# Kernel tuning notes

Hardware: AMD Instinct MI355X
Metric: run time of the kernel (lower is better)

The kernel has to match this reference:

```python
import jax, jax.numpy as jnp
import numpy as np
from jax import lax

C = 768
CA = C // 4  # adapter_channels = 192
L = 197      # 1 CLS + 14*14 patches
T_FRAMES = 16
B = 16
N = B * T_FRAMES


def quick_gelu(x):
    return x * jax.nn.sigmoid(1.702 * x)


def setup_inputs() -> dict:
    key = jax.random.key(0)
    ks = jax.random.split(key, 16)
    s = 0.02
    return {
        "x": jax.random.normal(ks[0], (L, N, C), dtype=jnp.float32),
        "T": T_FRAMES,
        # main path (fc1 -> depthwise conv1d over T -> fc2)
        "fc1_w": jax.random.normal(ks[1], (C, CA), jnp.float32) * s,
        "fc1_b": jnp.zeros((CA,), jnp.float32),
        "conv_w": jax.random.normal(ks[2], (CA, 1, 3), jnp.float32) * s,  # (O, I/g, K)
        "conv_b": jnp.zeros((CA,), jnp.float32),
        "fc2_w": jax.random.normal(ks[3], (CA, C), jnp.float32) * s,
        "fc2_b": jnp.zeros((C,), jnp.float32),
        # offset adapter (fc1 -> depthwise conv3d (1,3,3) -> fc2)
        "off_fc1_w": jax.random.normal(ks[4], (C, CA), jnp.float32) * s,
        "off_fc1_b": jnp.zeros((CA,), jnp.float32),
        "off_conv_w": jax.random.normal(ks[5], (CA, 1, 1, 3, 3), jnp.float32) * s,  # (O, I/g, D, H, W)
        "off_conv_b": jnp.zeros((CA,), jnp.float32),
        "off_fc2_w": jax.random.normal(ks[6], (CA, C), jnp.float32) * s,
        "off_fc2_b": jnp.zeros((C,), jnp.float32),
        # mlp branch (c_in -> QuickGELU -> c_out)
        "mlp_in_w": jax.random.normal(ks[7], (C, CA), jnp.float32) * s,
        "mlp_in_b": jnp.zeros((CA,), jnp.float32),
        "mlp_out_w": jax.random.normal(ks[8], (CA, C), jnp.float32) * s,
        "mlp_out_b": jnp.zeros((C,), jnp.float32),
    }


def _offset_adapter(x, T, fc1_w, fc1_b, conv_w, conv_b, fc2_w, fc2_b):
    Lx, Nx, Cx = x.shape
    Bx = Nx // T
    HW = Lx - 1
    H = int(round(HW ** 0.5))
    Ca = fc1_w.shape[1]
    xp = jnp.transpose(x, (1, 0, 2))            # (N, L, C)
    xs = xp[:, 1:, :].reshape(Bx, T, HW, Cx)    # (B, T, HW, C)
    # former frame: index [0, 0, 1, ..., T-2]
    x_former = jnp.concatenate([xs[:, :1], xs[:, :-1]], axis=1)
    off = xs - x_former
    off = off @ fc1_w + fc1_b                   # (B, T, HW, Ca)
    off = off.reshape(Bx, T, H, H, Ca).transpose(0, 4, 1, 2, 3)  # (B, Ca, T, H, W)
    off = lax.conv_general_dilated(
        off, conv_w, window_strides=(1, 1, 1),
        padding=[(0, 0), (1, 1), (1, 1)],
        dimension_numbers=("NCDHW", "OIDHW", "NCDHW"),
        feature_group_count=Ca,
    ) + conv_b[None, :, None, None, None]
    off = off.transpose(0, 2, 3, 4, 1).reshape(Nx, HW, Ca)
    off = off @ fc2_w + fc2_b                   # (N, L-1, C)
    return jnp.transpose(off, (1, 0, 2))        # (L-1, N, C)


def reference(x, T, fc1_w, fc1_b, conv_w, conv_b, fc2_w, fc2_b,
              off_fc1_w, off_fc1_b, off_conv_w, off_conv_b, off_fc2_w, off_fc2_b,
              mlp_in_w, mlp_in_b, mlp_out_w, mlp_out_b):
    Lx, Nx, Cx = x.shape
    Bx = Nx // T
    Ca = fc1_w.shape[1]

    offset = _offset_adapter(x, T, off_fc1_w, off_fc1_b, off_conv_w, off_conv_b,
                             off_fc2_w, off_fc2_b)  # (L-1, N, C)

    # mlp identity branch
    x_id = quick_gelu(x @ mlp_in_w + mlp_in_b) @ mlp_out_w + mlp_out_b  # (L, N, C)

    # main branch: fc1 -> depthwise conv1d along T -> fc2
    h = x @ fc1_w + fc1_b                                   # (L, N, Ca)
    h = jnp.transpose(h, (1, 0, 2)).reshape(Bx, T, Lx, Ca)  # (B, T, L, Ca)
    h = h.transpose(0, 2, 3, 1).reshape(Bx * Lx, Ca, T)     # (B*L, Ca, T)
    h = lax.conv_general_dilated(
        h, conv_w, window_strides=(1,), padding=[(1, 1)],
        dimension_numbers=("NCH", "OIH", "NCH"),
        feature_group_count=Ca,
    ) + conv_b[None, :, None]
    h = h.transpose(0, 2, 1).reshape(Bx, Lx, T, Ca)
    h = h.transpose(0, 2, 1, 3).reshape(Nx, Lx, Ca)
    h = jnp.transpose(h, (1, 0, 2))                         # (L, N, Ca)
    h = h @ fc2_w + fc2_b                                   # (L, N, C)

    x_id = x_id.at[1:].add(offset)
    return h + x_id
```

## Files before the change

kernel.cpp:

```cpp
#include <hip/hip_runtime.h>

#define L_DIM 197
#define N_DIM 256
#define C_DIM 768
#define CA_DIM 192
#define M_DIM (L_DIM * N_DIM)

typedef short s16x8 __attribute__((ext_vector_type(8)));
typedef float f32x4 __attribute__((ext_vector_type(4)));

__device__ __forceinline__ unsigned short f2bf(float f) {
  unsigned x = __builtin_bit_cast(unsigned, f);
  x = (x + 0x7fffu + ((x >> 16) & 1u)) >> 16;
  return (unsigned short)x;
}
__device__ __forceinline__ float bflo(unsigned u) { return __builtin_bit_cast(float, u << 16); }
__device__ __forceinline__ float bfhi(unsigned u) { return __builtin_bit_cast(float, u & 0xffff0000u); }

__device__ __forceinline__ void unp8(uint4 v, float* f) {
  f[0] = bflo(v.x); f[1] = bfhi(v.x); f[2] = bflo(v.y); f[3] = bfhi(v.y);
  f[4] = bflo(v.z); f[5] = bfhi(v.z); f[6] = bflo(v.w); f[7] = bfhi(v.w);
}

__device__ __forceinline__ void mfma16(f32x4& acc, s16x8 a, s16x8 b) {
  asm("v_mfma_f32_16x16x32_bf16 %0, %1, %2, %0" : "+v"(acc) : "v"(a), "v"(b));
}

typedef const void __attribute__((address_space(1)))* gp_t;
typedef void __attribute__((address_space(3)))* lp_t;
__device__ __forceinline__ void gl16(const void* g, void* l) {
  __builtin_amdgcn_global_load_lds((gp_t)g, (lp_t)l, 16, 0, 0);
}

#define WAITVM(n) asm volatile("s_waitcnt vmcnt(" #n ")" ::: "memory")

__device__ __forceinline__ int swz(int pid, int nwg) {
  const int q = nwg >> 3, r = nwg & 7, x = pid & 7, s = pid >> 3;
  return (x < r ? x * (q + 1) : r * (q + 1) + (x - r) * q) + s;
}

__global__ __launch_bounds__(256) void prep_k(
    const float* __restrict__ fc1_w, const float* __restrict__ mlp_in_w,
    const float* __restrict__ off_fc1_w, const float* __restrict__ fc2_w,
    const float* __restrict__ mlp_out_w, const float* __restrict__ off_fc2_w,
    unsigned short* __restrict__ wa, unsigned short* __restrict__ wc) {
  __shared__ float t[32][33];
  const int b = blockIdx.x;
  const int job = b / 144, tt = b - job * 144;
  const float* in = job == 0 ? fc1_w : job == 1 ? mlp_in_w : job == 2 ? off_fc1_w
                  : job == 3 ? fc2_w : job == 4 ? mlp_out_w : off_fc2_w;
  const int Cc = job < 3 ? 192 : 768;
  const int tc = Cc >> 5;
  const int tr0 = (tt / tc) << 5, tc0 = (tt - (tt / tc) * tc) << 5;
  const int lr = threadIdx.x >> 5, lc = threadIdx.x & 31;
#pragma unroll
  for (int p = 0; p < 4; p++)
    t[p * 8 + lr][lc] = in[(tr0 + p * 8 + lr) * Cc + tc0 + lc];
  __syncthreads();
#pragma unroll
  for (int p = 0; p < 4; p++) {
    const int orow = tc0 + p * 8 + lr;
    const int ocol = tr0 + lc;
    const unsigned short v = f2bf(t[lc][p * 8 + lr]);
    if (job < 3) wa[(job * 192 + orow) * 768 + ocol] = v;
    else         wc[orow * 576 + (job - 3) * 192 + ocol] = v;
  }
}

__global__ __launch_bounds__(256) void xcvt_k(const float* __restrict__ x,
                                              unsigned short* __restrict__ xb) {
  const int total8 = M_DIM * C_DIM / 8;
  const int step = gridDim.x * 256;
  for (int i = blockIdx.x * 256 + threadIdx.x; i < total8; i += step) {
    const float4 a = *(const float4*)(x + (size_t)i * 8);
    const float4 b = *(const float4*)(x + (size_t)i * 8 + 4);
    s16x8 v;
    v[0] = (short)f2bf(a.x); v[1] = (short)f2bf(a.y);
    v[2] = (short)f2bf(a.z); v[3] = (short)f2bf(a.w);
    v[4] = (short)f2bf(b.x); v[5] = (short)f2bf(b.y);
    v[6] = (short)f2bf(b.z); v[7] = (short)f2bf(b.w);
    *(s16x8*)(xb + (size_t)i * 8) = v;
  }
}

__global__ __launch_bounds__(256, 1) void gemm_a_k(
    const unsigned short* __restrict__ xb, const unsigned short* __restrict__ wa,
    const float* __restrict__ fc1_b, const float* __restrict__ mlp_in_b,
    const float* __restrict__ cw, const float* __restrict__ cb,
    const float* __restrict__ off_b1, unsigned short* __restrict__ hcat) {
  __shared__ unsigned short As[3][128 * 32];
  __shared__ unsigned short Bs[3][192 * 32];
  const int tid = threadIdx.x, lane = tid & 63, w = tid >> 6;
  const int lid = swz(blockIdx.x, 3 * 394);
  const int by = lid / 3, bx = lid - by * 3;
  const int m0 = by * 128, n0 = bx * 192;

  const int sr = tid >> 2, sc = (tid & 3) * 8;
  const unsigned short* gA0 = xb + (size_t)(m0 + sr) * C_DIM + sc;
  const unsigned short* gA1 = xb + (size_t)(m0 + 64 + sr) * C_DIM + sc;
  const unsigned short* gB = wa + (size_t)(n0 + sr) * C_DIM + sc;

  auto stage = [&](int kt, int b) {
    gl16(gA0 + kt * 32, &As[b][sr * 32 + sc]);
    gl16(gA1 + kt * 32, &As[b][(64 + sr) * 32 + sc]);
    const unsigned short* pb = gB + kt * 32;
    gl16(pb,               &Bs[b][sr * 32 + sc]);
    gl16(pb + 64 * C_DIM,  &Bs[b][(64 + sr) * 32 + sc]);
    gl16(pb + 128 * C_DIM, &Bs[b][(128 + sr) * 32 + sc]);
  };

  f32x4 acc[4][6];
#pragma unroll
  for (int i = 0; i < 4; i++)
#pragma unroll
    for (int j = 0; j < 6; j++) acc[i][j] = (f32x4){0.f, 0.f, 0.f, 0.f};

  const int fr = lane & 15, fq = lane >> 4;
  const int wm = (w >> 1) * 64, wn = (w & 1) * 96;

  stage(0, 0);
#pragma unroll 3
  for (int kt = 0; kt < 24; ++kt) {
    const int b = kt % 3;
    if (kt + 1 < 24) { stage(kt + 1, (kt + 1) % 3); WAITVM(5); }
    else             { WAITVM(0); }
    __builtin_amdgcn_s_barrier();
    asm volatile("" ::: "memory");
    s16x8 af[4], bfv[6];
#pragma unroll
    for (int mi = 0; mi < 4; mi++)
      af[mi] = *(const s16x8*)&As[b][(wm + mi * 16 + fr) * 32 + fq * 8];
#pragma unroll
    for (int ni = 0; ni < 6; ni++)
      bfv[ni] = *(const s16x8*)&Bs[b][(wn + ni * 16 + fr) * 32 + fq * 8];
#pragma unroll
    for (int mi = 0; mi < 4; mi++)
#pragma unroll
      for (int ni = 0; ni < 6; ni++) mfma16(acc[mi][ni], af[mi], bfv[ni]);
  }

  if (bx == 0) {
#pragma unroll
    for (int ni = 0; ni < 6; ni++) {
      const int ca = wn + ni * 16 + fr;
      const float bv = fc1_b[ca];
      const float w0 = cw[ca * 3], w1 = cw[ca * 3 + 1], w2 = cw[ca * 3 + 2];
      const float cbv = cb[ca];
#pragma unroll
      for (int mi = 0; mi < 4; mi++) {
        const float v0 = acc[mi][ni][0] + bv, v1 = acc[mi][ni][1] + bv;
        const float v2 = acc[mi][ni][2] + bv, v3 = acc[mi][ni][3] + bv;
        const float pv3 = __shfl_up(v3, 16);
        const float nv0 = __shfl_down(v0, 16);
        const float p0 = fq > 0 ? pv3 : 0.f;
        const float n3 = fq < 3 ? nv0 : 0.f;
        const int mb = m0 + wm + mi * 16 + fq * 4;
        hcat[(size_t)(mb + 0) * 576 + ca] = f2bf(w0 * p0 + w1 * v0 + w2 * v1 + cbv);
        hcat[(size_t)(mb + 1) * 576 + ca] = f2bf(w0 * v0 + w1 * v1 + w2 * v2 + cbv);
        hcat[(size_t)(mb + 2) * 576 + ca] = f2bf(w0 * v1 + w1 * v2 + w2 * v3 + cbv);
        hcat[(size_t)(mb + 3) * 576 + ca] = f2bf(w0 * v2 + w1 * v3 + w2 * n3 + cbv);
      }
    }
  } else if (bx == 1) {
#pragma unroll
    for (int ni = 0; ni < 6; ni++) {
      const int ca = wn + ni * 16 + fr;
      const float bv = mlp_in_b[ca];
#pragma unroll
      for (int mi = 0; mi < 4; mi++)
#pragma unroll
        for (int r = 0; r < 4; r++) {
          const int m = m0 + wm + mi * 16 + fq * 4 + r;
          float v = acc[mi][ni][r] + bv;
          v = v / (1.f + __expf(-1.702f * v));
          hcat[(size_t)m * 576 + 192 + ca] = f2bf(v);
        }
    }
  } else {
    const bool zrow = (by < 2);
#pragma unroll
    for (int ni = 0; ni < 6; ni++) {
      const int ca = wn + ni * 16 + fr;
      const float bv = off_b1[ca];
#pragma unroll
      for (int mi = 0; mi < 4; mi++) {
        const float v0 = acc[mi][ni][0], v1 = acc[mi][ni][1];
        const float v2 = acc[mi][ni][2], v3 = acc[mi][ni][3];
        const float pv3 = __shfl_up(v3, 16);
        const int mb = m0 + wm + mi * 16 + fq * 4;
        const float o0 = (fq == 0) ? bv : (v0 - pv3 + bv);
        if (zrow) {
          hcat[(size_t)(mb + 0) * 576 + 384 + ca] = 0;
          hcat[(size_t)(mb + 1) * 576 + 384 + ca] = 0;
          hcat[(size_t)(mb + 2) * 576 + 384 + ca] = 0;
          hcat[(size_t)(mb + 3) * 576 + 384 + ca] = 0;
        } else {
          hcat[(size_t)(mb + 0) * 576 + 384 + ca] = f2bf(o0);
          hcat[(size_t)(mb + 1) * 576 + 384 + ca] = f2bf(v1 - v0 + bv);
          hcat[(size_t)(mb + 2) * 576 + 384 + ca] = f2bf(v2 - v1 + bv);
          hcat[(size_t)(mb + 3) * 576 + 384 + ca] = f2bf(v3 - v2 + bv);
        }
      }
    }
  }
}

__global__ __launch_bounds__(256) void conv3d_k(
    const float* __restrict__ w3, const float* __restrict__ b2,
    unsigned short* __restrict__ hcat) {
  __shared__ float ds[196 * 48];
  __shared__ float w3s[9 * 48];
  __shared__ float b2s[48];
  const int blk = blockIdx.x;
  const int n = blk >> 2, q = blk & 3;
  const int ch0 = q * 48;
  const int tid = threadIdx.x;

  for (int j = tid; j < 432; j += 256) {
    const int c = j / 9, tap = j % 9;
    w3s[tap * 48 + c] = w3[(ch0 + c) * 9 + tap];
  }
  if (tid < 48) b2s[tid] = b2[ch0 + tid];

  for (int j = tid; j < 196 * 6; j += 256) {
    const int hw = j / 6, ck = j % 6;
    float dv[8];
    unp8(*(const uint4*)(hcat + ((size_t)(1 + hw) * 256 + n) * 576 + 384 + ch0 + ck * 8), dv);
#pragma unroll
    for (int e = 0; e < 8; e++) ds[hw * 48 + ck * 8 + e] = dv[e];
  }
  __syncthreads();

  for (int j = tid; j < 196 * 6; j += 256) {
    const int hw = j / 6, ck = j % 6;
    const int i = hw / 14, j0 = hw - i * 14;
    float acc[8];
#pragma unroll
    for (int e = 0; e < 8; e++) acc[e] = b2s[ck * 8 + e];
#pragma unroll
    for (int di = 0; di < 3; di++) {
      const int ii = i + di - 1;
      if (ii < 0 || ii >= 14) continue;
#pragma unroll
      for (int dj = 0; dj < 3; dj++) {
        const int jc = j0 + dj - 1;
        if (jc < 0 || jc >= 14) continue;
        const float* dp = &ds[(ii * 14 + jc) * 48 + ck * 8];
        const float* wp = &w3s[(di * 3 + dj) * 48 + ck * 8];
#pragma unroll
        for (int e = 0; e < 8; e++) acc[e] += wp[e] * dp[e];
      }
    }
    unsigned o[4];
#pragma unroll
    for (int e = 0; e < 8; e += 2)
      o[e / 2] = (unsigned)f2bf(acc[e]) | ((unsigned)f2bf(acc[e + 1]) << 16);
    uint4 ov; ov.x = o[0]; ov.y = o[1]; ov.z = o[2]; ov.w = o[3];
    *(uint4*)(hcat + ((size_t)(1 + hw) * 256 + n) * 576 + 384 + ch0 + ck * 8) = ov;
  }
}

__global__ __launch_bounds__(256, 1) void gemm_c_k(
    const unsigned short* __restrict__ hcat, const unsigned short* __restrict__ wc,
    const float* __restrict__ fc2_b, const float* __restrict__ mlp_out_b,
    const float* __restrict__ off_fc2_b, float* __restrict__ out) {
  __shared__ unsigned short As[3][128 * 32];
  __shared__ unsigned short Bs[3][128 * 32];
  const int tid = threadIdx.x, lane = tid & 63, w = tid >> 6;
  const int lid = swz(blockIdx.x, 6 * 394);
  const int by = lid / 6, bx = lid - by * 6;
  const int m0 = by * 128, n0 = bx * 128;

  const int srow = w * 32 + (lane >> 2), sc = (lane & 3) << 3;
  const unsigned short* gA = hcat + (size_t)(m0 + srow) * 576 + sc;
  const unsigned short* gB = wc + (size_t)(n0 + srow) * 576 + sc;
  auto stage = [&](int kt, int b) {
#pragma unroll
    for (int j = 0; j < 2; j++) {
      gl16(gA + kt * 32 + j * 16 * 576, &As[b][(srow + j * 16) * 32 + sc]);
      gl16(gB + kt * 32 + j * 16 * 576, &Bs[b][(srow + j * 16) * 32 + sc]);
    }
  };

  f32x4 acc[4][4];
#pragma unroll
  for (int i = 0; i < 4; i++)
#pragma unroll
    for (int j = 0; j < 4; j++) acc[i][j] = (f32x4){0.f, 0.f, 0.f, 0.f};

  const int fr = lane & 15, fq = lane >> 4;
  const int wm = (w >> 1) * 64, wn = (w & 1) * 64;

  stage(0, 0);
#pragma unroll 3
  for (int kt = 0; kt < 18; ++kt) {
    const int b = kt % 3;
    if (kt + 1 < 18) { stage(kt + 1, (kt + 1) % 3); WAITVM(4); }
    else             { WAITVM(0); }
    __builtin_amdgcn_s_barrier();
    asm volatile("" ::: "memory");
    s16x8 af[4], bfv[4];
#pragma unroll
    for (int mi = 0; mi < 4; mi++)
      af[mi] = *(const s16x8*)&As[b][(wm + mi * 16 + fr) * 32 + fq * 8];
#pragma unroll
    for (int ni = 0; ni < 4; ni++)
      bfv[ni] = *(const s16x8*)&Bs[b][(wn + ni * 16 + fr) * 32 + fq * 8];
#pragma unroll
    for (int mi = 0; mi < 4; mi++)
#pragma unroll
      for (int ni = 0; ni < 4; ni++) mfma16(acc[mi][ni], af[mi], bfv[ni]);
  }

  float bv[4];
#pragma unroll
  for (int ni = 0; ni < 4; ni++) {
    const int c = n0 + wn + ni * 16 + fr;
    bv[ni] = fc2_b[c] + mlp_out_b[c] + (by >= 2 ? off_fc2_b[c] : 0.f);
  }
#pragma unroll
  for (int mi = 0; mi < 4; mi++)
#pragma unroll
    for (int r = 0; r < 4; r++) {
      const int m = m0 + wm + mi * 16 + fq * 4 + r;
      float* op = out + (size_t)m * C_DIM + n0 + wn;
#pragma unroll
      for (int ni = 0; ni < 4; ni++) op[ni * 16 + fr] = acc[mi][ni][r] + bv[ni];
    }
}

extern "C" void kernel_launch(void* const* d_in, const int* in_sizes, int n_in,
                              void* d_out, int out_size, void* d_ws, size_t ws_size,
                              hipStream_t stream) {
  const float* x          = (const float*)d_in[0];
  const float* fc1_w      = (const float*)d_in[2];
  const float* fc1_b      = (const float*)d_in[3];
  const float* conv_w     = (const float*)d_in[4];
  const float* conv_b     = (const float*)d_in[5];
  const float* fc2_w      = (const float*)d_in[6];
  const float* fc2_b      = (const float*)d_in[7];
  const float* off_fc1_w  = (const float*)d_in[8];
  const float* off_fc1_b  = (const float*)d_in[9];
  const float* off_conv_w = (const float*)d_in[10];
  const float* off_conv_b = (const float*)d_in[11];
  const float* off_fc2_w  = (const float*)d_in[12];
  const float* off_fc2_b  = (const float*)d_in[13];
  const float* mlp_in_w   = (const float*)d_in[14];
  const float* mlp_in_b   = (const float*)d_in[15];
  const float* mlp_out_w  = (const float*)d_in[16];
  const float* mlp_out_b  = (const float*)d_in[17];
  float* out = (float*)d_out;

  char* ws = (char*)d_ws;
  unsigned short* xb   = (unsigned short*)(ws);
  unsigned short* hcat = (unsigned short*)(ws + (size_t)M_DIM * C_DIM * 2);
  unsigned short* wa   = (unsigned short*)(ws + (size_t)M_DIM * C_DIM * 2
                                              + (size_t)M_DIM * 576 * 2);
  unsigned short* wc   = wa + (size_t)576 * 768;

  prep_k<<<864, 256, 0, stream>>>(fc1_w, mlp_in_w, off_fc1_w, fc2_w, mlp_out_w,
                                  off_fc2_w, wa, wc);
  xcvt_k<<<2048, 256, 0, stream>>>(x, xb);
  gemm_a_k<<<1182, 256, 0, stream>>>(xb, wa, fc1_b, mlp_in_b, conv_w, conv_b,
                                     off_fc1_b, hcat);
  conv3d_k<<<1024, 256, 0, stream>>>(off_conv_w, off_conv_b, hcat);
  gemm_c_k<<<2364, 256, 0, stream>>>(hcat, wc, fc2_b, mlp_out_b, off_fc2_b, out);
}
```

Baseline: 217.0 us.

## Fuse fp32-to-bf16 conversion into GEMM A loader and widen GEMM C tiles

Removes the separate x conversion kernel. The first GEMM now loads fp32 x through registers, converts it with packed bf16 conversion instructions and writes it to LDS, using a two-set register prefetch pipeline. This avoids writing and rereading a bf16 copy of x, which is the largest tensor. The second GEMM's N tile widens from 128 to 256, halving the grid and raising per-wave accumulator count, which improves A reuse at the cost of register pressure.

```diff
diff --git a/kernel.cpp b/kernel.cpp
--- a/kernel.cpp
+++ b/kernel.cpp
@@ -22,6 +22,12 @@
   f[4] = bflo(v.z); f[5] = bfhi(v.z); f[6] = bflo(v.w); f[7] = bfhi(v.w);
 }
 
+__device__ __forceinline__ unsigned cvtpk(float lo, float hi) {
+  unsigned r;
+  asm("v_cvt_pk_bf16_f32 %0, %1, %2" : "=v"(r) : "v"(lo), "v"(hi));
+  return r;
+}
+
 __device__ __forceinline__ void mfma16(f32x4& acc, s16x8 a, s16x8 b) {
   asm("v_mfma_f32_16x16x32_bf16 %0, %1, %2, %0" : "+v"(acc) : "v"(a), "v"(b));
 }
@@ -33,6 +39,7 @@
 }
 
 #define WAITVM(n) asm volatile("s_waitcnt vmcnt(" #n ")" ::: "memory")
+#define BARRIER_LG() asm volatile("s_waitcnt lgkmcnt(0)\ns_barrier" ::: "memory")
 
 __device__ __forceinline__ int swz(int pid, int nwg) {
   const int q = nwg >> 3, r = nwg & 7, x = pid & 7, s = pid >> 3;
@@ -67,24 +74,8 @@
   }
 }
 
-__global__ __launch_bounds__(256) void xcvt_k(const float* __restrict__ x,
-                                              unsigned short* __restrict__ xb) {
-  const int total8 = M_DIM * C_DIM / 8;
-  const int step = gridDim.x * 256;
-  for (int i = blockIdx.x * 256 + threadIdx.x; i < total8; i += step) {
-    const float4 a = *(const float4*)(x + (size_t)i * 8);
-    const float4 b = *(const float4*)(x + (size_t)i * 8 + 4);
-    s16x8 v;
-    v[0] = (short)f2bf(a.x); v[1] = (short)f2bf(a.y);
-    v[2] = (short)f2bf(a.z); v[3] = (short)f2bf(a.w);
-    v[4] = (short)f2bf(b.x); v[5] = (short)f2bf(b.y);
-    v[6] = (short)f2bf(b.z); v[7] = (short)f2bf(b.w);
-    *(s16x8*)(xb + (size_t)i * 8) = v;
-  }
-}
-
 __global__ __launch_bounds__(256, 1) void gemm_a_k(
-    const unsigned short* __restrict__ xb, const unsigned short* __restrict__ wa,
+    const float* __restrict__ x, const unsigned short* __restrict__ wa,
     const float* __restrict__ fc1_b, const float* __restrict__ mlp_in_b,
     const float* __restrict__ cw, const float* __restrict__ cb,
     const float* __restrict__ off_b1, unsigned short* __restrict__ hcat) {
@@ -95,18 +86,30 @@
   const int by = lid / 3, bx = lid - by * 3;
   const int m0 = by * 128, n0 = bx * 192;
 
-  const int sr = tid >> 2, sc = (tid & 3) * 8;
-  const unsigned short* gA0 = xb + (size_t)(m0 + sr) * C_DIM + sc;
-  const unsigned short* gA1 = xb + (size_t)(m0 + 64 + sr) * C_DIM + sc;
-  const unsigned short* gB = wa + (size_t)(n0 + sr) * C_DIM + sc;
-
-  auto stage = [&](int kt, int b) {
-    gl16(gA0 + kt * 32, &As[b][sr * 32 + sc]);
-    gl16(gA1 + kt * 32, &As[b][(64 + sr) * 32 + sc]);
+  const int sr = tid >> 2, sc8 = (tid & 3) * 8;
+  const float* gA = x + (size_t)(m0 + sr) * C_DIM + sc8;
+  const unsigned short* gB = wa + (size_t)(n0 + sr) * C_DIM + sc8;
+
+  float4 avA[4], avB[4];
+  auto ldA = [&](int kt, float4* av) {
+    const float* p = gA + kt * 32;
+    av[0] = *(const float4*)p;                  av[1] = *(const float4*)(p + 4);
+    av[2] = *(const float4*)(p + 64 * C_DIM);   av[3] = *(const float4*)(p + 64 * C_DIM + 4);
+  };
+  auto wrA = [&](int b, const float4* av) {
+    uint4 u0, u1;
+    u0.x = cvtpk(av[0].x, av[0].y); u0.y = cvtpk(av[0].z, av[0].w);
+    u0.z = cvtpk(av[1].x, av[1].y); u0.w = cvtpk(av[1].z, av[1].w);
+    u1.x = cvtpk(av[2].x, av[2].y); u1.y = cvtpk(av[2].z, av[2].w);
+    u1.z = cvtpk(av[3].x, av[3].y); u1.w = cvtpk(av[3].z, av[3].w);
+    *(uint4*)&As[b][sr * 32 + sc8] = u0;
+    *(uint4*)&As[b][(64 + sr) * 32 + sc8] = u1;
+  };
+  auto stB = [&](int kt, int b) {
     const unsigned short* pb = gB + kt * 32;
-    gl16(pb,               &Bs[b][sr * 32 + sc]);
-    gl16(pb + 64 * C_DIM,  &Bs[b][(64 + sr) * 32 + sc]);
-    gl16(pb + 128 * C_DIM, &Bs[b][(128 + sr) * 32 + sc]);
+    gl16(pb,               &Bs[b][sr * 32 + sc8]);
+    gl16(pb + 64 * C_DIM,  &Bs[b][(64 + sr) * 32 + sc8]);
+    gl16(pb + 128 * C_DIM, &Bs[b][(128 + sr) * 32 + sc8]);
   };
 
   f32x4 acc[4][6];
@@ -118,14 +121,24 @@
   const int fr = lane & 15, fq = lane >> 4;
   const int wm = (w >> 1) * 64, wn = (w & 1) * 96;
 
-  stage(0, 0);
-#pragma unroll 3
+  ldA(0, avA);
+  stB(0, 0);
+  ldA(1, avB);
+  WAITVM(7);
+  wrA(0, avA);
+
+#pragma unroll 6
   for (int kt = 0; kt < 24; ++kt) {
     const int b = kt % 3;
-    if (kt + 1 < 24) { stage(kt + 1, (kt + 1) % 3); WAITVM(5); }
-    else             { WAITVM(0); }
-    __builtin_amdgcn_s_barrier();
-    asm volatile("" ::: "memory");
+    float4* ldset = ((kt & 1) == 0) ? avA : avB;
+    float4* wrset = ((kt & 1) == 0) ? avB : avA;
+    if (kt + 2 < 24) ldA(kt + 2, ldset);
+    if (kt + 1 < 24) stB(kt + 1, (kt + 1) % 3);
+    if (kt < 22)      { WAITVM(7); }
+    else if (kt == 22){ WAITVM(3); }
+    else              { WAITVM(0); }
+    if (kt + 1 < 24) wrA((kt + 1) % 3, wrset);
+    BARRIER_LG();
     s16x8 af[4], bfv[6];
 #pragma unroll
     for (int mi = 0; mi < 4; mi++)
@@ -265,56 +278,57 @@
     const float* __restrict__ fc2_b, const float* __restrict__ mlp_out_b,
     const float* __restrict__ off_fc2_b, float* __restrict__ out) {
   __shared__ unsigned short As[3][128 * 32];
-  __shared__ unsigned short Bs[3][128 * 32];
+  __shared__ unsigned short Bs[3][256 * 32];
   const int tid = threadIdx.x, lane = tid & 63, w = tid >> 6;
-  const int lid = swz(blockIdx.x, 6 * 394);
-  const int by = lid / 6, bx = lid - by * 6;
-  const int m0 = by * 128, n0 = bx * 128;
-
-  const int srow = w * 32 + (lane >> 2), sc = (lane & 3) << 3;
-  const unsigned short* gA = hcat + (size_t)(m0 + srow) * 576 + sc;
-  const unsigned short* gB = wc + (size_t)(n0 + srow) * 576 + sc;
+  const int lid = swz(blockIdx.x, 3 * 394);
+  const int by = lid / 3, bx = lid - by * 3;
+  const int m0 = by * 128, n0 = bx * 256;
+
+  const int sr = tid >> 2, sc = (tid & 3) * 8;
+  const unsigned short* gA = hcat + (size_t)(m0 + sr) * 576 + sc;
+  const unsigned short* gB = wc + (size_t)(n0 + sr) * 576 + sc;
   auto stage = [&](int kt, int b) {
 #pragma unroll
-    for (int j = 0; j < 2; j++) {
-      gl16(gA + kt * 32 + j * 16 * 576, &As[b][(srow + j * 16) * 32 + sc]);
-      gl16(gB + kt * 32 + j * 16 * 576, &Bs[b][(srow + j * 16) * 32 + sc]);
-    }
+    for (int j = 0; j < 2; j++)
+      gl16(gA + kt * 32 + j * 64 * 576, &As[b][(sr + j * 64) * 32 + sc]);
+#pragma unroll
+    for (int j = 0; j < 4; j++)
+      gl16(gB + kt * 32 + j * 64 * 576, &Bs[b][(sr + j * 64) * 32 + sc]);
   };
 
-  f32x4 acc[4][4];
+  f32x4 acc[4][8];
 #pragma unroll
   for (int i = 0; i < 4; i++)
 #pragma unroll
-    for (int j = 0; j < 4; j++) acc[i][j] = (f32x4){0.f, 0.f, 0.f, 0.f};
+    for (int j = 0; j < 8; j++) acc[i][j] = (f32x4){0.f, 0.f, 0.f, 0.f};
 
   const int fr = lane & 15, fq = lane >> 4;
-  const int wm = (w >> 1) * 64, wn = (w & 1) * 64;
+  const int wm = (w >> 1) * 64, wn = (w & 1) * 128;
 
   stage(0, 0);
 #pragma unroll 3
   for (int kt = 0; kt < 18; ++kt) {
     const int b = kt % 3;
-    if (kt + 1 < 18) { stage(kt + 1, (kt + 1) % 3); WAITVM(4); }
+    if (kt + 1 < 18) { stage(kt + 1, (kt + 1) % 3); WAITVM(6); }
     else             { WAITVM(0); }
     __builtin_amdgcn_s_barrier();
     asm volatile("" ::: "memory");
-    s16x8 af[4], bfv[4];
+    s16x8 af[4], bfv[8];
 #pragma unroll
     for (int mi = 0; mi < 4; mi++)
       af[mi] = *(const s16x8*)&As[b][(wm + mi * 16 + fr) * 32 + fq * 8];
 #pragma unroll
-    for (int ni = 0; ni < 4; ni++)
+    for (int ni = 0; ni < 8; ni++)
       bfv[ni] = *(const s16x8*)&Bs[b][(wn + ni * 16 + fr) * 32 + fq * 8];
 #pragma unroll
     for (int mi = 0; mi < 4; mi++)
 #pragma unroll
-      for (int ni = 0; ni < 4; ni++) mfma16(acc[mi][ni], af[mi], bfv[ni]);
-  }
-
-  float bv[4];
-#pragma unroll
-  for (int ni = 0; ni < 4; ni++) {
+      for (int ni = 0; ni < 8; ni++) mfma16(acc[mi][ni], af[mi], bfv[ni]);
+  }
+
+  float bv[8];
+#pragma unroll
+  for (int ni = 0; ni < 8; ni++) {
     const int c = n0 + wn + ni * 16 + fr;
     bv[ni] = fc2_b[c] + mlp_out_b[c] + (by >= 2 ? off_fc2_b[c] : 0.f);
   }
@@ -325,7 +339,7 @@
       const int m = m0 + wm + mi * 16 + fq * 4 + r;
       float* op = out + (size_t)m * C_DIM + n0 + wn;
 #pragma unroll
-      for (int ni = 0; ni < 4; ni++) op[ni * 16 + fr] = acc[mi][ni][r] + bv[ni];
+      for (int ni = 0; ni < 8; ni++) op[ni * 16 + fr] = acc[mi][ni][r] + bv[ni];
     }
 }
 
@@ -352,17 +366,14 @@
   float* out = (float*)d_out;
 
   char* ws = (char*)d_ws;
-  unsigned short* xb   = (unsigned short*)(ws);
-  unsigned short* hcat = (unsigned short*)(ws + (size_t)M_DIM * C_DIM * 2);
-  unsigned short* wa   = (unsigned short*)(ws + (size_t)M_DIM * C_DIM * 2
-                                              + (size_t)M_DIM * 576 * 2);
+  unsigned short* hcat = (unsigned short*)(ws);
+  unsigned short* wa   = (unsigned short*)(ws + (size_t)M_DIM * 576 * 2);
   unsigned short* wc   = wa + (size_t)576 * 768;
 
   prep_k<<<864, 256, 0, stream>>>(fc1_w, mlp_in_w, off_fc1_w, fc2_w, mlp_out_w,
                                   off_fc2_w, wa, wc);
-  xcvt_k<<<2048, 256, 0, stream>>>(x, xb);
-  gemm_a_k<<<1182, 256, 0, stream>>>(xb, wa, fc1_b, mlp_in_b, conv_w, conv_b,
+  gemm_a_k<<<1182, 256, 0, stream>>>(x, wa, fc1_b, mlp_in_b, conv_w, conv_b,
                                      off_fc1_b, hcat);
   conv3d_k<<<1024, 256, 0, stream>>>(off_conv_w, off_conv_b, hcat);
-  gemm_c_k<<<2364, 256, 0, stream>>>(hcat, wc, fc2_b, mlp_out_b, off_fc2_b, out);
-}
+  gemm_c_k<<<1182, 256, 0, stream>>>(hcat, wc, fc2_b, mlp_out_b, off_fc2_b, out);
+}
```

New measurement: 204.1 us. 6.0% less time.
